# Optimization experiments

Measured on AMD Instinct MI355X. Metric: run time of the kernel, lower is better.

Reference implementation:

```python
import jax, jax.numpy as jnp
import numpy as np

BATCH, SEQ, D_MODEL = 8, 4096, 1024
N, K, RHO_MAX, N_POWER_ITER = 16, 4, 0.3, 2
P = N * (N - 1) // 2  # 120 skew params


def _xavier(key, shape, gain):
    fan_out, fan_in = shape
    std = gain * np.sqrt(2.0 / (fan_in + fan_out))
    return jax.random.normal(key, shape, jnp.float32) * std


def setup_inputs() -> dict:
    key = jax.random.key(0)
    k0, k1, k2, k3 = jax.random.split(key, 4)
    u = jax.random.normal(k0, (BATCH, SEQ, D_MODEL), jnp.float32)
    W_proj_w = _xavier(k1, (P, D_MODEL), 0.1)
    W_proj_b = jnp.zeros((P,), jnp.float32)
    B_w = _xavier(k2, (N, D_MODEL), 0.5)
    C_w = _xavier(k3, (D_MODEL, N), 0.5)
    D = jnp.zeros((D_MODEL,), jnp.float32)
    return {"u": u, "W_proj_w": W_proj_w, "W_proj_b": W_proj_b, "B_w": B_w, "C_w": C_w, "D": D}


def _normalize(x, axis):
    # F.normalize: x / max(||x||, eps)
    return x / jnp.maximum(jnp.linalg.norm(x, axis=axis, keepdims=True), 1e-12)


def reference(u, W_proj_w, W_proj_b, B_w, C_w, D):
    Bsz, T, d = u.shape
    n = B_w.shape[0]
    rows, cols = np.triu_indices(n, 1)

    # 1. skew params for all timesteps at once: (B,T,P)
    v = u @ W_proj_w.T + W_proj_b
    A = jnp.zeros((Bsz, T, n, n), u.dtype)
    A = A.at[..., rows, cols].set(v).at[..., cols, rows].set(-v)

    # 2. spectral-norm scaling (power iteration runs with no grad in torch)
    A_sg = jax.lax.stop_gradient(A)
    u_vec = _normalize(jax.random.normal(jax.random.key(1), (Bsz, T, n, 1), u.dtype), axis=2)
    for _ in range(N_POWER_ITER):
        v_vec = _normalize(jnp.swapaxes(A_sg, -1, -2) @ u_vec, axis=2)
        u_vec = _normalize(A_sg @ v_vec, axis=2)
    sigma = jnp.abs((jnp.swapaxes(u_vec, -1, -2) @ (A @ v_vec))[..., 0, 0])  # (B,T)
    scale = RHO_MAX / jnp.maximum(sigma, RHO_MAX)
    A = A * scale[..., None, None]

    # 3. Neumann-Cayley, k=4 radix-2 splitting: W = (I-A)(I+A^2)(I-A)
    I = jnp.eye(n, dtype=u.dtype)
    ImA = I - A
    W = (ImA @ (I + A @ A)) @ ImA  # (B,T,n,n)

    # orthogonality deviation (monitoring, no grad)
    W_sg = jax.lax.stop_gradient(W)
    WtW = jnp.swapaxes(W_sg, -1, -2) @ W_sg
    ortho_dev = jnp.mean(jnp.linalg.norm(WtW - I, axis=(-2, -1)))

    # 4. sequential state recurrence h_t = W_t h_{t-1} + B u_t via scan
    Bx = u @ B_w.T  # (B,T,n)

    def step(h, inp):
        W_t, bx_t = inp  # (B,n,n), (B,n)
        h = jnp.einsum('bij,bj->bi', W_t, h) + bx_t
        return h, h

    h0 = jnp.zeros((Bsz, n), u.dtype)
    _, hs = jax.lax.scan(step, h0, (jnp.swapaxes(W, 0, 1), jnp.swapaxes(Bx, 0, 1)))
    h_all = jnp.swapaxes(hs, 0, 1)  # (B,T,n)

    y = h_all @ C_w.T + u * D
    return y, ortho_dev
```

## Files before the change

kernel.cpp:

```cpp
#include <hip/hip_runtime.h>
#include <hip/hip_bf16.h>
#include <math.h>

#define BATCHN 8
#define SEQN 4096
#define DMODEL 1024
#define MTOT (BATCHN*SEQN)
#define VB_STRIDE 136
#define CHUNKS 128
#define CLEN 32
#define YSIZE ((size_t)MTOT*DMODEL)
#define BN_ROWS 144
#define K1_UNITS 1152

typedef __attribute__((ext_vector_type(8))) short short8;
typedef __attribute__((ext_vector_type(4))) float f32x4;

__device__ __forceinline__ unsigned short f2bf(float x){
  __hip_bfloat16 h = __float2bfloat16(x);
  return *(unsigned short*)&h;
}
__device__ __forceinline__ float bf2f(unsigned short b){
  __hip_bfloat16 h; *(unsigned short*)&h = b;
  return __bfloat162float(h);
}

__device__ __forceinline__ void gload16(unsigned short* lds, const unsigned short* g){
  __builtin_amdgcn_global_load_lds(
      (const __attribute__((address_space(1))) unsigned int*)g,
      (__attribute__((address_space(3))) unsigned int*)lds,
      16, 0, 0);
}

__device__ __forceinline__ void wave_sync(){
  __builtin_amdgcn_sched_barrier(0);
  asm volatile("s_waitcnt lgkmcnt(0)" ::: "memory");
  __builtin_amdgcn_sched_barrier(0);
}

__device__ __forceinline__ unsigned rotl32(unsigned x, int d){ return (x<<d)|(x>>(32-d)); }
__device__ __forceinline__ void tfr(unsigned &x0, unsigned &x1, int r){ x0 += x1; x1 = rotl32(x1,r); x1 ^= x0; }

__device__ __forceinline__ float xla_erfinv(float x){
  float w = -log1pf(-x*x);
  float p;
  if (w < 5.0f){
    w = w - 2.5f;
    p = 2.81022636e-08f;
    p = fmaf(p, w, 3.43273939e-07f);
    p = fmaf(p, w, -3.5233877e-06f);
    p = fmaf(p, w, -4.39150654e-06f);
    p = fmaf(p, w, 0.00021858087f);
    p = fmaf(p, w, -0.00125372503f);
    p = fmaf(p, w, -0.00417768164f);
    p = fmaf(p, w, 0.246640727f);
    p = fmaf(p, w, 1.50140941f);
  } else {
    w = sqrtf(w) - 3.0f;
    p = -0.000200214257f;
    p = fmaf(p, w, 0.000100950558f);
    p = fmaf(p, w, 0.00134934322f);
    p = fmaf(p, w, -0.00367342844f);
    p = fmaf(p, w, 0.00573950773f);
    p = fmaf(p, w, -0.0076224613f);
    p = fmaf(p, w, 0.00943887047f);
    p = fmaf(p, w, 1.00167406f);
    p = fmaf(p, w, 2.83297682f);
  }
  return p * x;
}

__device__ float jax_randn(unsigned I){
  unsigned x0 = 0u, x1 = I;
  const unsigned ks2 = 0x1BD11BDBu;
  x0 += 0u; x1 += 1u;
  tfr(x0,x1,13); tfr(x0,x1,15); tfr(x0,x1,26); tfr(x0,x1,6);
  x0 += 1u; x1 += ks2 + 1u;
  tfr(x0,x1,17); tfr(x0,x1,29); tfr(x0,x1,16); tfr(x0,x1,24);
  x0 += ks2; x1 += 0u + 2u;
  tfr(x0,x1,13); tfr(x0,x1,15); tfr(x0,x1,26); tfr(x0,x1,6);
  x0 += 0u; x1 += 1u + 3u;
  tfr(x0,x1,17); tfr(x0,x1,29); tfr(x0,x1,16); tfr(x0,x1,24);
  x0 += 1u; x1 += ks2 + 4u;
  tfr(x0,x1,13); tfr(x0,x1,15); tfr(x0,x1,26); tfr(x0,x1,6);
  x0 += ks2; x1 += 0u + 5u;
  unsigned bits = x0 ^ x1;
  unsigned fb = (bits >> 9) | 0x3f800000u;
  float f = __uint_as_float(fb) - 1.0f;
  const float lo = -0.99999994f;
  float val = f * 2.0f + lo;
  val = fmaxf(lo, val);
  return 1.4142135381698608f * xla_erfinv(val);
}

__global__ __launch_bounds__(256) void k0_presplit(const float* __restrict__ Wp,
    const float* __restrict__ Bw, unsigned short* __restrict__ Bfrag){
  int i = blockIdx.x*256 + threadIdx.x;
  if (i >= BN_ROWS*DMODEL/4) return;
  int n = i >> 8;
  int k = (i & 255) * 4;
  float4 t4 = make_float4(0.f,0.f,0.f,0.f);
  if (n < 120)      t4 = *(const float4*)(Wp + (size_t)n*DMODEL + k);
  else if (n < 136) t4 = *(const float4*)(Bw + (size_t)(n-120)*DMODEL + k);
  unsigned short h[4], l[4];
  float v[4] = {t4.x,t4.y,t4.z,t4.w};
  #pragma unroll
  for (int j=0;j<4;j++){
    h[j] = f2bf(v[j]);
    l[j] = f2bf(v[j] - bf2f(h[j]));
  }
  int c  = k >> 5;
  int q  = (k >> 3) & 3;
  int jj = k & 7;
  size_t base = (size_t)c*K1_UNITS*8;
  *(ushort4*)(Bfrag + base + (size_t)(n*4+q)*8 + jj)        = make_ushort4(h[0],h[1],h[2],h[3]);
  *(ushort4*)(Bfrag + base + (size_t)((n+144)*4+q)*8 + jj)  = make_ushort4(l[0],l[1],l[2],l[3]);
}

#define K1_THREADS 512

#define K1_STAGE(C, BUF) do{                                                   \
  const unsigned short* _gB = Bfrag + (size_t)(C)*(K1_UNITS*8);                \
  unsigned short* _l = &Bs[BUF][0];                                            \
  gload16(_l + (wid*64)*8,      _gB + (size_t)(tid)*8);                        \
  gload16(_l + (wid*64+512)*8,  _gB + (size_t)(tid+512)*8);                    \
  if (wid < 2)                                                                 \
    gload16(_l + (wid*64+1024)*8, _gB + (size_t)(tid+1024)*8);                 \
}while(0)

#define K1_ALOAD(C, ARA, ARB) do{                                              \
  const float* _ap = aptr + (C)*32;                                            \
  ARA = *(const float4*)(_ap);                                                 \
  ARB = *(const float4*)(_ap + 4);                                             \
}while(0)

#define K1_COMPUTE(BUF, ARA, ARB) do{                                          \
  short8 _ah, _al;                                                             \
  {                                                                            \
    float _va[8] = {ARA.x,ARA.y,ARA.z,ARA.w,ARB.x,ARB.y,ARB.z,ARB.w};          \
    _Pragma("unroll")                                                          \
    for (int _j=0;_j<8;_j++){                                                  \
      unsigned short _h = f2bf(_va[_j]);                                       \
      _ah[_j] = (short)_h;                                                     \
      _al[_j] = (short)f2bf(_va[_j] - bf2f(_h));                               \
    }                                                                          \
  }                                                                            \
  const unsigned short* _sb = &Bs[BUF][0];                                     \
  _Pragma("unroll")                                                            \
  for (int _t=0;_t<5;_t++){                                                    \
    if (_t < nt){                                                              \
      int _row = (t0+_t)*16 + lrow;                                            \
      short8 _bh = *(const short8*)(_sb + _row*32 + quad*8);                   \
      short8 _bl = *(const short8*)(_sb + (_row+144)*32 + quad*8);             \
      acc[_t] = __builtin_amdgcn_mfma_f32_16x16x32_bf16(_ah, _bh, acc[_t], 0,0,0); \
      acc[_t] = __builtin_amdgcn_mfma_f32_16x16x32_bf16(_ah, _bl, acc[_t], 0,0,0); \
      acc[_t] = __builtin_amdgcn_mfma_f32_16x16x32_bf16(_al, _bh, acc[_t], 0,0,0); \
    }                                                                          \
  }                                                                            \
}while(0)

__global__ __launch_bounds__(512, 4) void k1_mfma(const float* __restrict__ u,
    const unsigned short* __restrict__ Bfrag,
    const float* __restrict__ Wpb, float* __restrict__ vb){
  __shared__ unsigned short Bs[2][K1_UNITS*8];

  const int tid  = threadIdx.x;
  const int wid  = tid >> 6;
  const int lane = tid & 63;
  const int quad = lane >> 4;
  const int lrow = lane & 15;
  const int wm   = wid & 3;
  const int wn   = wid >> 2;
  const int t0   = wn ? 5 : 0;
  const int nt   = wn ? 4 : 5;
  const int m0   = blockIdx.x * 64;

  const float* aptr = u + (size_t)(m0 + wm*16 + lrow)*DMODEL + quad*8;

  f32x4 acc[5];
  #pragma unroll
  for (int t=0;t<5;t++) acc[t] = (f32x4){0.f,0.f,0.f,0.f};

  float4 a0a, a0b, a1a, a1b;

  K1_STAGE(0, 0);
  K1_ALOAD(0, a0a, a0b);
  __syncthreads();

  for (int c=0; c<DMODEL/32; c+=2){
    K1_STAGE(c+1, 1);
    K1_ALOAD(c+1, a1a, a1b);
    K1_COMPUTE(0, a0a, a0b);
    __syncthreads();
    if (c+2 < DMODEL/32){
      K1_STAGE(c+2, 0);
      K1_ALOAD(c+2, a0a, a0b);
    }
    K1_COMPUTE(1, a1a, a1b);
    if (c+2 < DMODEL/32) __syncthreads();
  }

  #pragma unroll
  for (int t=0;t<5;t++){
    if (t < nt){
      int col = (t0+t)*16 + lrow;
      if (col < VB_STRIDE){
        float bias = (col < 120) ? Wpb[col] : 0.f;
        #pragma unroll
        for (int i=0;i<4;i++){
          int row = m0 + wm*16 + quad*4 + i;
          vb[(size_t)row*VB_STRIDE + col] = acc[t][i] + bias;
        }
      }
    }
  }
}

__global__ __launch_bounds__(128) void k2_build_w(const float* __restrict__ vb,
    float* __restrict__ Wg, float* __restrict__ ortho){
  __shared__ float Mf[8*324];
  __shared__ float gsum[8];
  const int tid = threadIdx.x;
  const int grp = tid >> 4;
  const int r   = tid & 15;
  const int m   = blockIdx.x*8 + grp;
  float* M = Mf + grp*324;
  const float* vrow = vb + (size_t)m*VB_STRIDE;

  float a_s[16];
  #pragma unroll
  for (int c=0;c<16;c++){
    float val = 0.f;
    if (c > r)      val =  vrow[r*15 - (r*(r-1))/2 + (c-r-1)];
    else if (c < r) val = -vrow[c*15 - (c*(c-1))/2 + (r-c-1)];
    a_s[c] = val;
  }

  float uv = jax_randn((unsigned)m*16u + (unsigned)r);
  float nn = uv*uv;
  #pragma unroll
  for (int s=1;s<16;s<<=1) nn += __shfl_xor(nn, s, 16);
  uv = uv / fmaxf(sqrtf(nn), 1e-12f);

  float t2 = 0.f;
  #pragma unroll
  for (int it=0; it<2; ++it){
    float t1 = 0.f;
    #pragma unroll
    for (int k=0;k<16;k++) t1 += a_s[k]*__shfl(uv, k, 16);
    t1 = -t1;
    nn = t1*t1;
    #pragma unroll
    for (int s=1;s<16;s<<=1) nn += __shfl_xor(nn, s, 16);
    float vvec = t1 / fmaxf(sqrtf(nn), 1e-12f);
    t2 = 0.f;
    #pragma unroll
    for (int k=0;k<16;k++) t2 += a_s[k]*__shfl(vvec, k, 16);
    nn = t2*t2;
    #pragma unroll
    for (int s=1;s<16;s<<=1) nn += __shfl_xor(nn, s, 16);
    uv = t2 / fmaxf(sqrtf(nn), 1e-12f);
  }
  float sig = uv * t2;
  #pragma unroll
  for (int s=1;s<16;s<<=1) sig += __shfl_xor(sig, s, 16);
  sig = fabsf(sig);
  const float scale = 0.3f / fmaxf(sig, 0.3f);
  #pragma unroll
  for (int k=0;k<16;k++) a_s[k] *= scale;

  #pragma unroll
  for (int q=0;q<4;q++)
    *(float4*)(M + r*20 + q*4) = make_float4(a_s[q*4],a_s[q*4+1],a_s[q*4+2],a_s[q*4+3]);
  wave_sync();

  float s_s[16];
  #pragma unroll
  for (int j=0;j<16;j++) s_s[j] = 0.f;
  #pragma unroll
  for (int k=0;k<16;k++){
    #pragma unroll
    for (int q=0;q<4;q++){
      float4 ak = *(const float4*)(M + k*20 + q*4);
      s_s[q*4+0] = fmaf(a_s[k], ak.x, s_s[q*4+0]);
      s_s[q*4+1] = fmaf(a_s[k], ak.y, s_s[q*4+1]);
      s_s[q*4+2] = fmaf(a_s[k], ak.z, s_s[q*4+2]);
      s_s[q*4+3] = fmaf(a_s[k], ak.w, s_s[q*4+3]);
    }
  }
  wave_sync();

  #pragma unroll
  for (int q=0;q<4;q++)
    *(float4*)(M + r*20 + q*4) = make_float4(s_s[q*4],s_s[q*4+1],s_s[q*4+2],s_s[q*4+3]);
  wave_sync();

  float c_s[16];
  #pragma unroll
  for (int j=0;j<16;j++) c_s[j] = 0.f;
  #pragma unroll
  for (int k=0;k<16;k++){
    float ck = s_s[k] - 2.f*a_s[k];
    #pragma unroll
    for (int q=0;q<4;q++){
      float4 sk = *(const float4*)(M + k*20 + q*4);
      c_s[q*4+0] = fmaf(ck, sk.x, c_s[q*4+0]);
      c_s[q*4+1] = fmaf(ck, sk.y, c_s[q*4+1]);
      c_s[q*4+2] = fmaf(ck, sk.z, c_s[q*4+2]);
      c_s[q*4+3] = fmaf(ck, sk.w, c_s[q*4+3]);
    }
  }
  float w_s[16];
  #pragma unroll
  for (int j=0;j<16;j++){
    float wv = -2.f*a_s[j] + 2.f*s_s[j] + c_s[j];
    if (j == r) wv += 1.f;
    w_s[j] = wv;
  }
  float4* wout = (float4*)(Wg + (size_t)m*256 + r*16);
  #pragma unroll
  for (int q=0;q<4;q++)
    wout[q] = make_float4(w_s[q*4],w_s[q*4+1],w_s[q*4+2],w_s[q*4+3]);
  wave_sync();

  #pragma unroll
  for (int q=0;q<4;q++)
    *(float4*)(M + r*20 + q*4) = make_float4(w_s[q*4],w_s[q*4+1],w_s[q*4+2],w_s[q*4+3]);
  wave_sync();
  float wt_s[16];
  #pragma unroll
  for (int j=0;j<16;j++) wt_s[j] = 0.f;
  #pragma unroll
  for (int k=0;k<16;k++){
    float ck = M[k*20 + r];
    #pragma unroll
    for (int q=0;q<4;q++){
      float4 wk = *(const float4*)(M + k*20 + q*4);
      wt_s[q*4+0] = fmaf(ck, wk.x, wt_s[q*4+0]);
      wt_s[q*4+1] = fmaf(ck, wk.y, wt_s[q*4+1]);
      wt_s[q*4+2] = fmaf(ck, wk.z, wt_s[q*4+2]);
      wt_s[q*4+3] = fmaf(ck, wk.w, wt_s[q*4+3]);
    }
  }
  float dev = 0.f;
  #pragma unroll
  for (int j=0;j<16;j++){
    float v = wt_s[j] - ((j==r)?1.f:0.f);
    dev += v*v;
  }
  #pragma unroll
  for (int s=1;s<16;s<<=1) dev += __shfl_xor(dev, s, 16);
  if (r==0) gsum[grp] = sqrtf(dev);
  __syncthreads();
  if (tid==0){
    float t=0.f;
    #pragma unroll
    for (int i=0;i<8;i++) t += gsum[i];
    atomicAdd(ortho, t);
  }
}

__global__ __launch_bounds__(64) void k3a_chunk_reduce(const float* __restrict__ Wg,
    const float* __restrict__ vb, double* __restrict__ Msum){
  const int chunk = blockIdx.x;
  const int b = chunk / CHUNKS, c = chunk - b*CHUNKS;
  const int lane = threadIdx.x, r = lane & 15, g = lane >> 4;
  __shared__ double Mb[2][16*20];
  __shared__ double sb[16];
  #pragma unroll
  for (int cc=0;cc<4;cc++) Mb[0][r*20 + 4*g + cc] = (r == 4*g+cc) ? 1.0 : 0.0;
  if (lane < 16) sb[lane] = 0.0;
  __syncthreads();
  const size_t mbase = (size_t)b*SEQN + (size_t)c*CLEN;
  float4 wq = *(const float4*)(Wg + mbase*256 + r*16 + 4*g);
  float bx = vb[mbase*VB_STRIDE + 120 + r];
  int p = 0;
  for (int t=0;t<CLEN;++t){
    float4 wn = make_float4(0.f,0.f,0.f,0.f); float bxn = 0.f;
    if (t+1 < CLEN){
      wn  = *(const float4*)(Wg + (mbase+t+1)*256 + r*16 + 4*g);
      bxn = vb[(mbase+t+1)*VB_STRIDE + 120 + r];
    }
    const double* M = Mb[p];
    double a0=0.0,a1=0.0,a2=0.0,a3=0.0, sacc=0.0;
    #pragma unroll
    for (int kg=0;kg<4;kg++){
      float wk0 = __shfl(wq.x, r + 16*kg);
      float wk1 = __shfl(wq.y, r + 16*kg);
      float wk2 = __shfl(wq.z, r + 16*kg);
      float wk3 = __shfl(wq.w, r + 16*kg);
      float wkv[4] = {wk0,wk1,wk2,wk3};
      #pragma unroll
      for (int e=0;e<4;e++){
        int k = 4*kg + e;
        double w = (double)wkv[e];
        const double* mrow = M + k*20 + 4*g;
        a0 = fma(w, mrow[0], a0);
        a1 = fma(w, mrow[1], a1);
        a2 = fma(w, mrow[2], a2);
        a3 = fma(w, mrow[3], a3);
        sacc = fma(w, sb[k], sacc);
      }
    }
    __syncthreads();
    double* Mn = Mb[1-p];
    Mn[r*20+4*g+0]=a0; Mn[r*20+4*g+1]=a1; Mn[r*20+4*g+2]=a2; Mn[r*20+4*g+3]=a3;
    if (g==0) sb[r] = sacc + (double)bx;
    __syncthreads();
    p ^= 1;
    wq = wn; bx = bxn;
  }
  double* out = Msum + (size_t)chunk*272;
  #pragma unroll
  for (int cc=0;cc<4;cc++) out[r*16+4*g+cc] = Mb[p][r*20+4*g+cc];
  if (lane<16) out[256+lane] = sb[lane];
}

__global__ __launch_bounds__(64) void k3b_prefix(const double* __restrict__ Msum,
    double* __restrict__ hstart){
  const int b = blockIdx.x;
  const int lane = threadIdx.x, r = lane & 15, g = lane >> 4;
  __shared__ double q[16];
  if (lane < 16) q[lane] = 0.0;
  __syncthreads();
  const double* base = Msum + (size_t)b*CHUNKS*272;
  double2 m01 = *(const double2*)(base + r*16 + 4*g);
  double2 m23 = *(const double2*)(base + r*16 + 4*g + 2);
  double sv = base[256 + r];
  for (int c=0;c<CHUNKS;++c){
    double2 n01, n23; double svn = 0.0;
    n01.x=n01.y=n23.x=n23.y=0.0;
    if (c+1 < CHUNKS){
      const double* bn = base + (size_t)(c+1)*272;
      n01 = *(const double2*)(bn + r*16 + 4*g);
      n23 = *(const double2*)(bn + r*16 + 4*g + 2);
      svn = bn[256 + r];
    }
    if (lane < 16) hstart[((size_t)b*CHUNKS + c)*16 + lane] = q[lane];
    double part = m01.x*q[4*g+0] + m01.y*q[4*g+1] + m23.x*q[4*g+2] + m23.y*q[4*g+3];
    part += __shfl_xor(part, 16);
    part += __shfl_xor(part, 32);
    __syncthreads();
    if (g==0) q[r] = part + sv;
    __syncthreads();
    m01 = n01; m23 = n23; sv = svn;
  }
}

__global__ __launch_bounds__(64) void k3c_apply(const float* __restrict__ Wg,
    const float* __restrict__ vb, const double* __restrict__ hstart,
    float* __restrict__ hout){
  const int chunk = blockIdx.x;
  const int b = chunk / CHUNKS, c = chunk - b*CHUNKS;
  const int lane = threadIdx.x, r = lane & 15, g = lane >> 4;
  __shared__ double h[16];
  if (lane < 16) h[lane] = hstart[(size_t)chunk*16 + lane];
  __syncthreads();
  const size_t mbase = (size_t)b*SEQN + (size_t)c*CLEN;
  float4 wq = *(const float4*)(Wg + mbase*256 + r*16 + 4*g);
  float bx = vb[mbase*VB_STRIDE + 120 + r];
  for (int t=0;t<CLEN;++t){
    float4 wn = make_float4(0.f,0.f,0.f,0.f); float bxn = 0.f;
    if (t+1 < CLEN){
      wn  = *(const float4*)(Wg + (mbase+t+1)*256 + r*16 + 4*g);
      bxn = vb[(mbase+t+1)*VB_STRIDE + 120 + r];
    }
    double part = (double)wq.x*h[4*g+0] + (double)wq.y*h[4*g+1]
                + (double)wq.z*h[4*g+2] + (double)wq.w*h[4*g+3];
    part += __shfl_xor(part, 16);
    part += __shfl_xor(part, 32);
    __syncthreads();
    if (g==0){
      double nh = part + (double)bx;
      h[r] = nh;
      hout[(mbase+t)*16 + r] = (float)nh;
    }
    __syncthreads();
    wq = wn; bx = bxn;
  }
}

__device__ __forceinline__ float dot4f(float4 a, float4 b){
  return a.x*b.x + a.y*b.y + a.z*b.z + a.w*b.w;
}

__global__ __launch_bounds__(256) void k4_out(const float* __restrict__ hbuf,
    const float* __restrict__ u, const float* __restrict__ Cw,
    const float* __restrict__ D, const float* __restrict__ ortho,
    float* __restrict__ y, int write_ortho){
  __shared__ float hl[256];
  const int m0 = blockIdx.x * 16;
  hl[threadIdx.x] = hbuf[(size_t)m0*16 + threadIdx.x];
  __syncthreads();
  const int col = threadIdx.x * 4;
  float4 cm[4][4];
  #pragma unroll
  for (int cc=0;cc<4;cc++)
    #pragma unroll
    for (int jj=0;jj<4;jj++)
      cm[cc][jj] = *(const float4*)(Cw + (size_t)(col+cc)*16 + jj*4);
  float4 d4 = *(const float4*)(D + col);
  #pragma unroll
  for (int row=0;row<16;row++){
    const float4* hr = (const float4*)(hl + row*16);
    float4 h0=hr[0], h1=hr[1], h2=hr[2], h3=hr[3];
    float4 o;
    o.x = dot4f(cm[0][0],h0)+dot4f(cm[0][1],h1)+dot4f(cm[0][2],h2)+dot4f(cm[0][3],h3);
    o.y = dot4f(cm[1][0],h0)+dot4f(cm[1][1],h1)+dot4f(cm[1][2],h2)+dot4f(cm[1][3],h3);
    o.z = dot4f(cm[2][0],h0)+dot4f(cm[2][1],h1)+dot4f(cm[2][2],h2)+dot4f(cm[2][3],h3);
    o.w = dot4f(cm[3][0],h0)+dot4f(cm[3][1],h1)+dot4f(cm[3][2],h2)+dot4f(cm[3][3],h3);
    size_t off = (size_t)(m0+row)*DMODEL + col;
    float4 u4 = *(const float4*)(u + off);
    o.x += u4.x*d4.x; o.y += u4.y*d4.y; o.z += u4.z*d4.z; o.w += u4.w*d4.w;
    *(float4*)(y + off) = o;
  }
  if (write_ortho && blockIdx.x==0 && threadIdx.x==0)
    y[YSIZE] = ortho[0] * (1.0f/32768.0f);
}

extern "C" void kernel_launch(void* const* d_in, const int* in_sizes, int n_in,
                              void* d_out, int out_size, void* d_ws, size_t ws_size,
                              hipStream_t stream){
  const float* u   = (const float*)d_in[0];
  const float* Wp  = (const float*)d_in[1];
  const float* Wpb = (const float*)d_in[2];
  const float* Bw  = (const float*)d_in[3];
  const float* Cw  = (const float*)d_in[4];
  const float* D   = (const float*)d_in[5];
  float* y = (float*)d_out;

  float* f      = (float*)d_ws;
  float* vb     = f;
  float* Wg     = vb  + (size_t)MTOT*VB_STRIDE;
  float* hbuf   = Wg  + (size_t)MTOT*256;
  double* Msum  = (double*)(hbuf + (size_t)MTOT*16);
  double* hstart= Msum + (size_t)BATCHN*CHUNKS*272;
  unsigned short* Bfrag = (unsigned short*)(hstart + (size_t)BATCHN*CHUNKS*16);
  float* ortho  = (float*)(Bfrag + (size_t)32*K1_UNITS*8);

  int write_ortho = ((size_t)out_size > YSIZE) ? 1 : 0;

  hipMemsetAsync(ortho, 0, sizeof(float), stream);
  hipLaunchKernelGGL(k0_presplit,     dim3((BN_ROWS*DMODEL/4+255)/256), dim3(256), 0, stream, Wp, Bw, Bfrag);
  hipLaunchKernelGGL(k1_mfma,         dim3(MTOT/64), dim3(K1_THREADS), 0, stream, u, Bfrag, Wpb, vb);
  hipLaunchKernelGGL(k2_build_w,      dim3(MTOT/8), dim3(128), 0, stream, vb, Wg, ortho);
  hipLaunchKernelGGL(k3a_chunk_reduce,dim3(BATCHN*CHUNKS), dim3(64), 0, stream, Wg, vb, Msum);
  hipLaunchKernelGGL(k3b_prefix,      dim3(BATCHN), dim3(64), 0, stream, Msum, hstart);
  hipLaunchKernelGGL(k3c_apply,       dim3(BATCHN*CHUNKS), dim3(64), 0, stream, Wg, vb, hstart, hbuf);
  hipLaunchKernelGGL(k4_out,          dim3(MTOT/16), dim3(256), 0, stream, hbuf, u, Cw, D, ortho, y, write_ortho);
}
```

Measured before the change: 462.6 us.

## Triple-buffer k1 B-fragment staging with explicit vmcnt fences

Moves the projection GEMM's shared-memory staging of B fragments from two buffers to three, so each chunk is prefetched two iterations ahead. Full __syncthreads are replaced by precise s_waitcnt vmcnt fences plus raw barriers, with sched_barriers around them. The per-warp load pattern is remapped so each wave stages a contiguous 144-unit slice. The aim is to keep global loads in flight across the barrier. In exchange it uses more LDS, which may lower occupancy, and the hand-counted vmcnt values are fragile.

```diff
diff --git a/kernel.cpp b/kernel.cpp
--- a/kernel.cpp
+++ b/kernel.cpp
@@ -121,17 +121,29 @@
 
 #define K1_STAGE(C, BUF) do{                                                   \
   const unsigned short* _gB = Bfrag + (size_t)(C)*(K1_UNITS*8);                \
-  unsigned short* _l = &Bs[BUF][0];                                            \
-  gload16(_l + (wid*64)*8,      _gB + (size_t)(tid)*8);                        \
-  gload16(_l + (wid*64+512)*8,  _gB + (size_t)(tid+512)*8);                    \
-  if (wid < 2)                                                                 \
-    gload16(_l + (wid*64+1024)*8, _gB + (size_t)(tid+1024)*8);                 \
+  unsigned short* _l = &Bs[0][0] + (size_t)(BUF)*(K1_UNITS*8);                 \
+  const int _u = wid*144;                                                      \
+  gload16(_l + (size_t)_u*8,        _gB + (size_t)(_u+lane)*8);                \
+  gload16(_l + (size_t)(_u+64)*8,   _gB + (size_t)(_u+64+lane)*8);             \
+  if (lane < 16)                                                               \
+    gload16(_l + (size_t)(_u+128)*8, _gB + (size_t)(_u+128+lane)*8);           \
 }while(0)
 
 #define K1_ALOAD(C, ARA, ARB) do{                                              \
   const float* _ap = aptr + (C)*32;                                            \
   ARA = *(const float4*)(_ap);                                                 \
   ARB = *(const float4*)(_ap + 4);                                             \
+}while(0)
+
+#define K1_FENCE(N) do{                                                       \
+  __builtin_amdgcn_sched_barrier(0);                                          \
+  asm volatile("s_waitcnt vmcnt(" #N ")" ::: "memory");                       \
+  __builtin_amdgcn_sched_barrier(0);                                          \
+}while(0)
+
+#define K1_BAR() do{                                                          \
+  __builtin_amdgcn_s_barrier();                                               \
+  __builtin_amdgcn_sched_barrier(0);                                          \
 }while(0)
 
 #define K1_COMPUTE(BUF, ARA, ARB) do{                                          \
@@ -145,7 +157,7 @@
       _al[_j] = (short)f2bf(_va[_j] - bf2f(_h));                               \
     }                                                                          \
   }                                                                            \
-  const unsigned short* _sb = &Bs[BUF][0];                                     \
+  const unsigned short* _sb = &Bs[0][0] + (size_t)(BUF)*(K1_UNITS*8);          \
   _Pragma("unroll")                                                            \
   for (int _t=0;_t<5;_t++){                                                    \
     if (_t < nt){                                                              \
@@ -162,7 +174,7 @@
 __global__ __launch_bounds__(512, 4) void k1_mfma(const float* __restrict__ u,
     const unsigned short* __restrict__ Bfrag,
     const float* __restrict__ Wpb, float* __restrict__ vb){
-  __shared__ unsigned short Bs[2][K1_UNITS*8];
+  __shared__ unsigned short Bs[3][K1_UNITS*8];
 
   const int tid  = threadIdx.x;
   const int wid  = tid >> 6;
@@ -185,19 +197,36 @@
 
   K1_STAGE(0, 0);
   K1_ALOAD(0, a0a, a0b);
-  __syncthreads();
-
+  K1_STAGE(1, 1);
+  K1_ALOAD(1, a1a, a1b);
+  K1_FENCE(5);
+  K1_BAR();
+
+  int cb0 = 0;
+  #pragma unroll 1
   for (int c=0; c<DMODEL/32; c+=2){
-    K1_STAGE(c+1, 1);
-    K1_ALOAD(c+1, a1a, a1b);
-    K1_COMPUTE(0, a0a, a0b);
-    __syncthreads();
+    const int bufc  = cb0;
+    const int bufn  = (cb0==2) ? 0 : cb0+1;
+    const int bufs0 = (cb0>=1) ? cb0-1 : 2;
+    K1_COMPUTE(bufc, a0a, a0b);
     if (c+2 < DMODEL/32){
-      K1_STAGE(c+2, 0);
+      K1_STAGE(c+2, bufs0);
       K1_ALOAD(c+2, a0a, a0b);
-    }
-    K1_COMPUTE(1, a1a, a1b);
-    if (c+2 < DMODEL/32) __syncthreads();
+      K1_FENCE(5);
+    } else {
+      K1_FENCE(0);
+    }
+    K1_BAR();
+    K1_COMPUTE(bufn, a1a, a1b);
+    if (c+3 < DMODEL/32){
+      K1_STAGE(c+3, bufc);
+      K1_ALOAD(c+3, a1a, a1b);
+      K1_FENCE(5);
+    } else {
+      K1_FENCE(0);
+    }
+    K1_BAR();
+    cb0 = bufs0;
   }
 
   #pragma unroll
```

After: 456.0 us. No clear change (-1.4%).
